# Kernel optimization log

Measured on AMD Instinct MI355X. Metric: run time of the kernel, lower is better.

## Reference

```python
import jax, jax.numpy as jnp
import numpy as np

KERNEL = (7, 7)
NUM_CH = 4
EPS = 1e-06
ROPE_BASE = 10000.0


def _rel_dist():
    coords = [np.arange(k, dtype=np.float32) - k // 2 for k in KERNEL]
    g = np.meshgrid(*coords, indexing='ij')
    d = np.sqrt(sum(gi ** 2 for gi in g))
    return jnp.asarray(d.reshape(-1)), float(d.max())


def silu(x):
    return x * jax.nn.sigmoid(x)


def rmsnorm(x, w):
    rms = jnp.sqrt(jnp.mean(x * x, axis=-1, keepdims=True) + EPS)
    return x / rms * w


def apply_rope(x):
    # x: (B, L, H, D); positions run over dim -2 (matches torch default)
    H, D = x.shape[-2], x.shape[-1]
    half = D // 2
    pos = jnp.arange(H, dtype=jnp.float32)
    freqs = 1.0 / (ROPE_BASE ** (jnp.arange(half, dtype=x.dtype) / half))
    ang = pos[:, None] * freqs  # (H, half)
    cos, sin = jnp.cos(ang), jnp.sin(ang)
    x1, x2 = x[..., :half], x[..., half:2 * half]
    return jnp.concatenate([x1 * cos - x2 * sin, x1 * sin + x2 * cos], axis=-1)


def unfold2d(x):
    # x: (B, Hs, Ws, C) -> (B, Hs, Ws, k1*k2, C), row-major kernel order
    B, Hs, Ws, C = x.shape
    k1, k2 = KERNEL
    xp = jnp.pad(x, ((0, 0), ((k1 - 1) // 2, k1 // 2), ((k2 - 1) // 2, k2 // 2), (0, 0)))
    wins = [xp[:, i:i + Hs, j:j + Ws, :] for i in range(k1) for j in range(k2)]
    return jnp.stack(wins, axis=3)


def setup_inputs() -> dict:
    key = jax.random.key(0)
    ks = jax.random.split(key, 8)
    C = 256
    x = jax.random.normal(ks[0], (2, 64, 64, C), dtype=jnp.float32)
    W_qkv = jax.random.normal(ks[1], (C, 3 * C), dtype=jnp.float32) * 0.02
    w_qnorm = jnp.ones((C // NUM_CH,), dtype=jnp.float32)
    w_knorm = jnp.ones((C // NUM_CH,), dtype=jnp.float32)
    W_wp = jax.random.normal(ks[2], (C, 2 * NUM_CH), dtype=jnp.float32) * 0.02
    b_wp = jax.random.normal(ks[3], (2 * NUM_CH,), dtype=jnp.float32) * 0.02
    w_onorm = jnp.ones((C,), dtype=jnp.float32)
    W_out = jax.random.normal(ks[4], (C, C), dtype=jnp.float32) * 0.02
    W_gate = jax.random.normal(ks[5], (C, C), dtype=jnp.float32) * 0.02
    b_gate = 2.0 * jnp.ones((C,), dtype=jnp.float32)
    return {"x": x, "W_qkv": W_qkv, "w_qnorm": w_qnorm, "w_knorm": w_knorm,
            "W_wp": W_wp, "b_wp": b_wp, "w_onorm": w_onorm, "W_out": W_out,
            "W_gate": W_gate, "b_gate": b_gate}


def reference(x, W_qkv, w_qnorm, w_knorm, W_wp, b_wp, w_onorm, W_out, W_gate, b_gate):
    rel_dist, max_dist = _rel_dist()
    B, Hs, Ws, C = x.shape
    L = Hs * Ws
    H = NUM_CH
    D = C // H
    Wsz = KERNEL[0] * KERNEL[1]
    scale = D ** (-0.5)

    qkv = silu(x @ W_qkv)
    q, k, v = jnp.split(qkv, 3, axis=-1)

    q_flat = apply_rope(rmsnorm(q.reshape(B, L, H, D), w_qnorm))
    k_flat = apply_rope(rmsnorm(k.reshape(B, L, H, D), w_knorm))
    k = k_flat.reshape(B, Hs, Ws, C)

    wp = silu(x @ W_wp + b_wp)  # (B, Hs, Ws, 2H)
    width_raw, sharp_raw = jnp.split(wp, 2, axis=-1)
    width = jax.nn.sigmoid(width_raw) * max_dist + 0.5
    sharpness = jax.nn.sigmoid(sharp_raw) * 9.5 + 0.5

    k_win = unfold2d(k).reshape(B, L, Wsz, H, D)
    v_win = unfold2d(v).reshape(B, L, Wsz, H, D)

    scores = jnp.einsum('blhd,blwhd->blhw', q_flat, k_win) * scale
    width_f = width.reshape(B, L, H, 1)
    sharp_f = sharpness.reshape(B, L, H, 1)
    soft_mask = jax.nn.sigmoid((width_f - rel_dist) * sharp_f)
    scores = scores - (1.0 - soft_mask) * 10000.0
    attn = jax.nn.softmax(scores, axis=-1)

    out = jnp.einsum('blhw,blwhd->blhd', attn, v_win).reshape(B, Hs, Ws, C)
    out = rmsnorm(out, w_onorm)

    gate = jax.nn.sigmoid(silu(v @ W_gate + b_gate))
    merged = gate * v + (1.0 - gate) * out
    return silu(merged @ W_out)
```

## Files before the change

kernel.cpp:

```cpp
#include <hip/hip_runtime.h>
#include <hip/hip_fp16.h>
#include <math.h>

__device__ __forceinline__ float sigm(float x)  { return 1.0f / (1.0f + __expf(-x)); }
__device__ __forceinline__ float siluf(float x) { return x * sigm(x); }

typedef _Float16 half8  __attribute__((ext_vector_type(8)));
typedef _Float16 half4  __attribute__((ext_vector_type(4)));
typedef float    f32x4  __attribute__((ext_vector_type(4)));

__device__ __forceinline__ void gld16(const void* g, void* l) {
    __builtin_amdgcn_global_load_lds(
        (const __attribute__((address_space(1))) unsigned*)g,
        (__attribute__((address_space(3))) unsigned*)l, 16, 0, 0);
}

template <int N>
__device__ __forceinline__ void wait_vmcnt() {
    if constexpr (N == 0)      asm volatile("s_waitcnt vmcnt(0)" ::: "memory");
    else if constexpr (N == 5) asm volatile("s_waitcnt vmcnt(5)" ::: "memory");
    else if constexpr (N == 6) asm volatile("s_waitcnt vmcnt(6)" ::: "memory");
}

template <int MI, int AMODE>
__device__ __forceinline__ void gemm_core16(
    const __half* __restrict__ A16,
    const __half* __restrict__ Bhi, const __half* __restrict__ Blo,
    int nbs, int m0, int n0, int t, f32x4 (&acc)[MI][4])
{
    __shared__ short As[2][MI * 1024], BsHi[2][4096], BsLo[2][4096];
    const int lane = t & 63, wave = t >> 6;
    const int wm = (wave >> 1) * (MI << 4), wn = (wave & 1) << 6;
    const int fr = lane & 15, fq = lane >> 4;
    constexpr int NL = MI / 2 + 4;

    auto stage = [&](int kb, int buf) {
#pragma unroll
        for (int hf = 0; hf < MI / 2; ++hf) {
            const int rr = wave * (MI << 3) + (hf << 4);
            size_t ga;
            if (AMODE == 0)
                ga = (((size_t)(kb * 8192 + m0 + rr)) << 5) + (lane << 3);
            else
                ga = (((size_t)(m0 + rr + (lane >> 2))) << 8) + (kb << 5) + ((lane & 3) << 3);
            gld16(A16 + ga, &As[buf][rr << 5]);
        }
#pragma unroll
        for (int hf = 0; hf < 2; ++hf) {
            const int rr = (wave << 5) + (hf << 4);
            const size_t gb = (((size_t)(kb * nbs + n0 + rr)) << 5) + (lane << 3);
            gld16(Bhi + gb, &BsHi[buf][rr << 5]);
            gld16(Blo + gb, &BsLo[buf][rr << 5]);
        }
    };

    stage(0, 0);
#pragma unroll
    for (int kb = 0; kb < 8; ++kb) {
        const int cur = kb & 1;
        if (kb < 7) {
            stage(kb + 1, cur ^ 1);
            wait_vmcnt<NL>();
        } else {
            wait_vmcnt<0>();
        }
        __builtin_amdgcn_s_barrier();

        half8 a[MI], bh[4], bl[4];
#pragma unroll
        for (int i = 0; i < MI; ++i)
            a[i] = *(const half8*)&As[cur][((wm + (i << 4) + fr) << 5) + (fq << 3)];
#pragma unroll
        for (int i = 0; i < 4; ++i) {
            const int boff = ((wn + (i << 4) + fr) << 5) + (fq << 3);
            bh[i] = *(const half8*)&BsHi[cur][boff];
            bl[i] = *(const half8*)&BsLo[cur][boff];
        }
#pragma unroll
        for (int mi = 0; mi < MI; ++mi)
#pragma unroll
            for (int ni = 0; ni < 4; ++ni) {
                acc[mi][ni] = __builtin_amdgcn_mfma_f32_16x16x32_f16(a[mi], bh[ni], acc[mi][ni], 0, 0, 0);
                acc[mi][ni] = __builtin_amdgcn_mfma_f32_16x16x32_f16(a[mi], bl[ni], acc[mi][ni], 0, 0, 0);
            }

        if (kb < 7) __builtin_amdgcn_s_barrier();
    }
}

__global__ __launch_bounds__(256) void prep_kernel(
    const float* __restrict__ x, const float* __restrict__ Wqkv,
    const float* __restrict__ Wgate, const float* __restrict__ Wout,
    const float* __restrict__ Wwp, const float* __restrict__ bwp,
    __half* __restrict__ xh,
    __half* __restrict__ wqh, __half* __restrict__ wql,
    __half* __restrict__ wgh, __half* __restrict__ wgl,
    __half* __restrict__ woh, __half* __restrict__ wol,
    float* __restrict__ width, float* __restrict__ sharp)
{
    __shared__ float xs[32][260];
    const int t = threadIdx.x;
    const int blk = blockIdx.x;
    if (blk < 256) {
        const int row0 = blk << 5;
        for (int e = t; e < 2048; e += 256) {
            int r = e >> 6, cc = (e & 63) << 2;
            *(float4*)&xs[r][cc] = *(const float4*)&x[(size_t)(row0 + r) * 256 + cc];
        }
        __syncthreads();
        const int r = t >> 3, kb = t & 7;
        __half hibuf[32];
#pragma unroll
        for (int i = 0; i < 32; ++i)
            hibuf[i] = __float2half(xs[r][(kb << 5) + i]);
        const size_t ob = ((size_t)(kb * 8192 + row0 + r)) << 5;
#pragma unroll
        for (int i = 0; i < 4; ++i)
            *(int4*)&xh[ob + (i << 3)] = *(int4*)&hibuf[i << 3];
        float a0 = 0.f, a1 = 0.f, a2 = 0.f, a3 = 0.f;
#pragma unroll 4
        for (int k = 0; k < 256; k += 4) {
            a0 += xs[r][k + 0] * Wwp[(k + 0) * 8 + kb];
            a1 += xs[r][k + 1] * Wwp[(k + 1) * 8 + kb];
            a2 += xs[r][k + 2] * Wwp[(k + 2) * 8 + kb];
            a3 += xs[r][k + 3] * Wwp[(k + 3) * 8 + kb];
        }
        const float acc = (a0 + a1) + (a2 + a3);
        float s = sigm(siluf(acc + bwp[kb]));
        const int row = row0 + r;
        if (kb < 4) width[row * 4 + kb] = s * 4.242640687119285f + 0.5f;
        else        sharp[row * 4 + kb - 4] = s * 9.5f + 0.5f;
    } else {
        const float* W; __half *Whi, *Wlo; int N, nb0, ncnt;
        if (blk < 288)      { W = Wqkv;  Whi = wqh; Wlo = wql; N = 768; nb0 = (blk - 256) * 24; ncnt = 24; }
        else if (blk < 296) { W = Wgate; Whi = wgh; Wlo = wgl; N = 256; nb0 = (blk - 288) * 32; ncnt = 32; }
        else                { W = Wout;  Whi = woh; Wlo = wol; N = 256; nb0 = (blk - 296) * 32; ncnt = 32; }
        for (int j = 0; j < ncnt; ++j)
            xs[j][t] = W[(size_t)t * N + nb0 + j];
        __syncthreads();
        for (int c = t; c < ncnt * 8; c += 256) {
            const int j = c >> 3, kb = c & 7;
            __half hibuf[32], lobuf[32];
#pragma unroll
            for (int i = 0; i < 32; ++i) {
                float v = xs[j][(kb << 5) + i];
                __half hv = __float2half(v);
                hibuf[i] = hv;
                lobuf[i] = __float2half(v - __half2float(hv));
            }
            const size_t ob = ((size_t)(kb * N + nb0 + j)) << 5;
#pragma unroll
            for (int i = 0; i < 4; ++i) {
                *(int4*)&Whi[ob + (i << 3)] = *(int4*)&hibuf[i << 3];
                *(int4*)&Wlo[ob + (i << 3)] = *(int4*)&lobuf[i << 3];
            }
        }
    }
}

__global__ __launch_bounds__(256, 3) void gemm_qkv(
    const __half* __restrict__ xh,
    const __half* __restrict__ wqh, const __half* __restrict__ wql,
    const float* __restrict__ wq, const float* __restrict__ wk,
    __half* __restrict__ qh, __half* __restrict__ kh, __half* __restrict__ vh)
{
    const int t  = threadIdx.x;
    const int m0 = blockIdx.y << 6, n0 = blockIdx.x << 7;
    f32x4 acc[2][4] = {};
    gemm_core16<2, 0>(xh, wqh, wql, 768, m0, n0, t, acc);

    const int lane = t & 63, wave = t >> 6;
    const int wm = (wave >> 1) << 5, wn = (wave & 1) << 6;
    const int fr = lane & 15, fq = lane >> 4;
    const int gc0 = n0 + wn;
    const int seg = gc0 >> 8;
    const int h   = (gc0 >> 6) & 3;
    const int hc0 = h << 6;

#pragma unroll
    for (int mi = 0; mi < 2; ++mi)
#pragma unroll
        for (int ni = 0; ni < 4; ++ni)
#pragma unroll
            for (int r = 0; r < 4; ++r)
                acc[mi][ni][r] = siluf(acc[mi][ni][r]);

    if (seg == 2) {
#pragma unroll
        for (int mi = 0; mi < 2; ++mi)
#pragma unroll
            for (int r = 0; r < 4; ++r) {
                const size_t row = m0 + wm + (mi << 4) + (fq << 2) + r;
#pragma unroll
                for (int ni = 0; ni < 4; ++ni)
                    vh[row * 256 + hc0 + (ni << 4) + fr] = __float2half(acc[mi][ni][r]);
            }
    } else {
        const float* wnorm = seg ? wk : wq;
        float wv[4];
#pragma unroll
        for (int ni = 0; ni < 4; ++ni) wv[ni] = wnorm[(ni << 4) + fr];
        float cs[2], sn[2];
#pragma unroll
        for (int j = 0; j < 2; ++j) {
            const int d = (j << 4) + fr;
            const float freq = powf(10000.f, -(float)d * (1.f / 32.f));
            const float ang = (float)h * freq;
            cs[j] = cosf(ang); sn[j] = sinf(ang);
        }
        __half* dstbase = (seg ? kh : qh);
#pragma unroll
        for (int mi = 0; mi < 2; ++mi)
#pragma unroll
            for (int r = 0; r < 4; ++r) {
                float ss = acc[mi][0][r] * acc[mi][0][r] + acc[mi][1][r] * acc[mi][1][r]
                         + acc[mi][2][r] * acc[mi][2][r] + acc[mi][3][r] * acc[mi][3][r];
                ss += __shfl_xor(ss, 1); ss += __shfl_xor(ss, 2);
                ss += __shfl_xor(ss, 4); ss += __shfl_xor(ss, 8);
                const float rinv = 1.f / sqrtf(ss * (1.f / 64.f) + 1e-6f);
                float xv[4];
#pragma unroll
                for (int ni = 0; ni < 4; ++ni) xv[ni] = acc[mi][ni][r] * rinv * wv[ni];
                const float o0 = xv[0] * cs[0] - xv[2] * sn[0];
                const float o2 = xv[0] * sn[0] + xv[2] * cs[0];
                const float o1 = xv[1] * cs[1] - xv[3] * sn[1];
                const float o3 = xv[1] * sn[1] + xv[3] * cs[1];
                const size_t row = m0 + wm + (mi << 4) + (fq << 2) + r;
                __half* dst = dstbase + row * 256 + hc0;
                dst[fr]      = __float2half(o0);
                dst[16 + fr] = __float2half(o1);
                dst[32 + fr] = __float2half(o2);
                dst[48 + fr] = __float2half(o3);
            }
    }
}

__global__ __launch_bounds__(256, 3) void gemm_gate(
    const __half* __restrict__ vh,
    const __half* __restrict__ wgh, const __half* __restrict__ wgl,
    const float* __restrict__ bias, const float* __restrict__ attn_o,
    const float* __restrict__ sumsq4, const float* __restrict__ w_onorm,
    __half* __restrict__ mh)
{
    const int t  = threadIdx.x;
    const int m0 = blockIdx.y << 6, n0 = blockIdx.x << 7;
    f32x4 acc[2][4] = {};
    gemm_core16<2, 1>(vh, wgh, wgl, 256, m0, n0, t, acc);

    const int lane = t & 63, wave = t >> 6;
    const int wm = (wave >> 1) << 5, wn = (wave & 1) << 6;
    const int fr = lane & 15, fq = lane >> 4;

    float rmsf[2][4];
#pragma unroll
    for (int mi = 0; mi < 2; ++mi)
#pragma unroll
        for (int r = 0; r < 4; ++r) {
            const int m = m0 + wm + (mi << 4) + (fq << 2) + r;
            float4 s4 = *(const float4*)&sumsq4[(size_t)m * 4];
            rmsf[mi][r] = 1.f / sqrtf((s4.x + s4.y + s4.z + s4.w) * (1.f / 256.f) + 1e-6f);
        }

#pragma unroll
    for (int mi = 0; mi < 2; ++mi)
#pragma unroll
        for (int ni = 0; ni < 4; ++ni) {
            const int n  = n0 + wn + (ni << 4) + fr;
            const int mb = m0 + wm + (mi << 4) + (fq << 2);
            const float bb  = bias[n];
            const float won = w_onorm[n];
#pragma unroll
            for (int r = 0; r < 4; ++r) {
                const int m = mb + r;
                const float g  = sigm(siluf(acc[mi][ni][r] + bb));
                const float vv = __half2float(vh[(size_t)m * 256 + n]);
                const float oo = attn_o[(size_t)m * 256 + n] * rmsf[mi][r] * won;
                mh[(size_t)m * 256 + n] = __float2half(g * vv + (1.f - g) * oo);
            }
        }
}

__global__ __launch_bounds__(256, 3) void gemm_out(
    const __half* __restrict__ mh,
    const __half* __restrict__ woh, const __half* __restrict__ wol,
    float* __restrict__ out)
{
    const int t  = threadIdx.x;
    const int m0 = blockIdx.y << 6, n0 = blockIdx.x << 7;
    f32x4 acc[2][4] = {};
    gemm_core16<2, 1>(mh, woh, wol, 256, m0, n0, t, acc);

    const int lane = t & 63, wave = t >> 6;
    const int wm = (wave >> 1) << 5, wn = (wave & 1) << 6;
    const int fr = lane & 15, fq = lane >> 4;
#pragma unroll
    for (int mi = 0; mi < 2; ++mi)
#pragma unroll
        for (int ni = 0; ni < 4; ++ni) {
            const int n  = n0 + wn + (ni << 4) + fr;
            const int mb = m0 + wm + (mi << 4) + (fq << 2);
#pragma unroll
            for (int r = 0; r < 4; ++r)
                out[(size_t)(mb + r) * 256 + n] = siluf(acc[mi][ni][r]);
        }
}

#define PT 216

__global__ __launch_bounds__(256, 2) void attn_mfma(
    const __half* __restrict__ qh, const __half* __restrict__ kh,
    const __half* __restrict__ vh, const float* __restrict__ width,
    const float* __restrict__ sharp, float* __restrict__ attn_o,
    float* __restrict__ sumsq4)
{
    __shared__ short smem[27648];
    short* Ksh = smem;
    short* Psh = smem;
    short* Vt  = smem + 13824;

    const int t = threadIdx.x;
    const int lane = t & 63, wave = t >> 6;
    const int fr = lane & 15, fq = lane >> 4;
    const int patch = blockIdx.x, h = blockIdx.y, b = blockIdx.z;
    const int pr0 = (patch >> 3) << 3, pc0 = (patch & 7) << 3;
    const int t0 = (wave * 28) >> 4;

    float wd[4], sh[4]; int lq[4];
#pragma unroll
    for (int r = 0; r < 4; ++r) {
        const int q = (wave << 4) + (fq << 2) + r;
        lq[r] = (pr0 + (q >> 3)) * 64 + pc0 + (q & 7);
        wd[r] = width[((b << 12) + lq[r]) * 4 + h];
        sh[r] = sharp[((b << 12) + lq[r]) * 4 + h];
    }

    const int qrow = (wave << 4) + fr;
    const int lqr = (pr0 + (qrow >> 3)) * 64 + pc0 + (qrow & 7);
    const __half* qptr = qh + (((size_t)(b << 12) + lqr) << 8) + (h << 6) + (fq << 3);
    half8 a0 = *(const half8*)qptr;
    half8 a1 = *(const half8*)(qptr + 32);

    const int srow = t >> 5;
    const int d2 = (t & 31) << 1;
    const size_t cbase = (((size_t)b << 12) * 256) + (size_t)h * 64 + d2;

    unsigned kb[25], vb[25];
#pragma unroll
    for (int p5 = 0; p5 < 25; ++p5) {
        const int prow = p5 * 8 + srow;
        const int pi = prow / 14, pj = prow - pi * 14;
        const int gr = pr0 - 3 + pi, gc = pc0 - 3 + pj;
        const bool ok = (prow < 196) & ((unsigned)gr < 64u) & ((unsigned)gc < 64u);
        const int grc = min(max(gr, 0), 63), gcc = min(max(gc, 0), 63);
        const size_t off = cbase + (size_t)(grc * 64 + gcc) * 256;
        unsigned kv = *(const unsigned*)(kh + off);
        unsigned vv = *(const unsigned*)(vh + off);
        kb[p5] = ok ? kv : 0u;
        vb[p5] = ok ? vv : 0u;
    }

    const int chunk = d2 >> 3, dlo = d2 & 7;
#pragma unroll
    for (int p5 = 0; p5 < 25; ++p5) {
        const int prow = p5 * 8 + srow;
        *(unsigned*)&Ksh[(prow << 6) + ((chunk ^ (prow & 7)) << 3) + dlo] = kb[p5];
        Vt[(d2)     * PT + prow] = (short)(vb[p5] & 0xffffu);
        Vt[(d2 + 1) * PT + prow] = (short)(vb[p5] >> 16);
    }
    if (t < 128) {
        const int rr = 200 + (t >> 4);
        *(unsigned*)&Ksh[(rr << 6) + (((t & 15) ^ ((rr & 7) << 1)) << 2)] = 0u;
    }
    for (int i = t; i < 64 * 20; i += 256)
        Vt[(i / 20) * PT + 196 + (i % 20)] = 0;
    __syncthreads();

    f32x4 sc[8];
#pragma unroll
    for (int tl = 0; tl < 8; ++tl) {
        const int kr = ((t0 + tl) << 4) + fr;
        half8 b0 = *(const half8*)&Ksh[(kr << 6) + (((0 + fq) ^ (kr & 7)) << 3)];
        half8 b1 = *(const half8*)&Ksh[(kr << 6) + (((4 + fq) ^ (kr & 7)) << 3)];
        f32x4 z = {0.f, 0.f, 0.f, 0.f};
        z = __builtin_amdgcn_mfma_f32_16x16x32_f16(a0, b0, z, 0, 0, 0);
        sc[tl] = __builtin_amdgcn_mfma_f32_16x16x32_f16(a1, b1, z, 0, 0, 0);
    }

    float mx[4] = {-3e38f, -3e38f, -3e38f, -3e38f};
#pragma unroll
    for (int tl = 0; tl < 8; ++tl) {
        const int p = ((t0 + tl) << 4) + fr;
        const int pi = p / 14, pj = p - pi * 14;
        const bool pvld = p < 196;
#pragma unroll
        for (int r = 0; r < 4; ++r) {
            const int q = (wave << 4) + (fq << 2) + r;
            const int di = pi - 3 - ((q >> 3) & 7), dj = pj - 3 - (q & 7);
            const bool win = pvld & ((unsigned)(di + 3) <= 6u) & ((unsigned)(dj + 3) <= 6u);
            const float rel = sqrtf((float)(di * di + dj * dj));
            const float mk = sigm((wd[r] - rel) * sh[r]);
            float s = sc[tl][r] * 0.125f - (1.f - mk) * 10000.f;
            s = win ? s : -3e38f;
            sc[tl][r] = s;
            mx[r] = fmaxf(mx[r], s);
        }
    }
#pragma unroll
    for (int r = 0; r < 4; ++r) {
        mx[r] = fmaxf(mx[r], __shfl_xor(mx[r], 1));
        mx[r] = fmaxf(mx[r], __shfl_xor(mx[r], 2));
        mx[r] = fmaxf(mx[r], __shfl_xor(mx[r], 4));
        mx[r] = fmaxf(mx[r], __shfl_xor(mx[r], 8));
    }
    float sm[4] = {0.f, 0.f, 0.f, 0.f};
#pragma unroll
    for (int tl = 0; tl < 8; ++tl)
#pragma unroll
        for (int r = 0; r < 4; ++r) {
            const float e = __expf(sc[tl][r] - mx[r]);
            sc[tl][r] = e; sm[r] += e;
        }
#pragma unroll
    for (int r = 0; r < 4; ++r) {
        sm[r] += __shfl_xor(sm[r], 1);
        sm[r] += __shfl_xor(sm[r], 2);
        sm[r] += __shfl_xor(sm[r], 4);
        sm[r] += __shfl_xor(sm[r], 8);
        sm[r] = 1.f / sm[r];
    }

    __syncthreads();
#pragma unroll
    for (int tl = 0; tl < 8; ++tl)
#pragma unroll
        for (int r = 0; r < 4; ++r) {
            __half pv = __float2half(sc[tl][r] * sm[r]);
            Psh[((wave << 4) + (fq << 2) + r) * PT + ((t0 + tl) << 4) + fr] = *(short*)&pv;
        }
    __syncthreads();

    f32x4 o[4] = {};
    const int pra = (wave << 4) + fr;
    const int cb = t0 << 4;
#pragma unroll
    for (int s = 0; s < 4; ++s) {
        half8 pa = *(const half8*)&Psh[pra * PT + cb + (fq << 3) + (s << 5)];
#pragma unroll
        for (int dt = 0; dt < 4; ++dt) {
            half8 vbf = *(const half8*)&Vt[((dt << 4) + fr) * PT + cb + (fq << 3) + (s << 5)];
            o[dt] = __builtin_amdgcn_mfma_f32_16x16x32_f16(pa, vbf, o[dt], 0, 0, 0);
        }
    }

#pragma unroll
    for (int r = 0; r < 4; ++r) {
        float ss = o[0][r]*o[0][r] + o[1][r]*o[1][r] + o[2][r]*o[2][r] + o[3][r]*o[3][r];
        ss += __shfl_xor(ss, 1); ss += __shfl_xor(ss, 2);
        ss += __shfl_xor(ss, 4); ss += __shfl_xor(ss, 8);
        const size_t rowb = (((size_t)(b << 12) + lq[r]) << 8) + h * 64;
#pragma unroll
        for (int dt = 0; dt < 4; ++dt)
            attn_o[rowb + (dt << 4) + fr] = o[dt][r];
        if (fr == 0) sumsq4[(((b << 12) + lq[r]) << 2) + h] = ss;
    }
}

extern "C" void kernel_launch(void* const* d_in, const int* in_sizes, int n_in,
                              void* d_out, int out_size, void* d_ws, size_t ws_size,
                              hipStream_t stream)
{
    const float* x      = (const float*)d_in[0];
    const float* W_qkv  = (const float*)d_in[1];
    const float* w_qn   = (const float*)d_in[2];
    const float* w_kn   = (const float*)d_in[3];
    const float* W_wp   = (const float*)d_in[4];
    const float* b_wp   = (const float*)d_in[5];
    const float* w_on   = (const float*)d_in[6];
    const float* W_out  = (const float*)d_in[7];
    const float* W_gate = (const float*)d_in[8];
    const float* b_gate = (const float*)d_in[9];
    float* out = (float*)d_out;

    __half* ws16 = (__half*)d_ws;
    __half* xh  = ws16;
    __half* wqh = xh  + 2097152;
    __half* wql = wqh + 196608;
    __half* wgh = wql + 196608;
    __half* wgl = wgh + 65536;
    __half* woh = wgl + 65536;
    __half* wol = woh + 65536;
    __half* qhp = wol + 65536;
    __half* khp = qhp + 2097152;
    __half* vhp = khp + 2097152;
    __half* mh  = vhp + 2097152;
    float* attn_o = (float*)(mh + 2097152);
    float* widthp = attn_o + 2097152;
    float* sharpp = widthp + 32768;
    float* sumsq4 = sharpp + 32768;

    prep_kernel<<<304, 256, 0, stream>>>(x, W_qkv, W_gate, W_out, W_wp, b_wp,
                                         xh, wqh, wql, wgh, wgl, woh, wol,
                                         widthp, sharpp);
    gemm_qkv<<<dim3(6, 128), 256, 0, stream>>>(xh, wqh, wql, w_qn, w_kn,
                                               qhp, khp, vhp);
    attn_mfma<<<dim3(64, 4, 2), 256, 0, stream>>>(qhp, khp, vhp, widthp, sharpp,
                                                  attn_o, sumsq4);
    gemm_gate<<<dim3(2, 128), 256, 0, stream>>>(vhp, wgh, wgl, b_gate,
                                                attn_o, sumsq4, w_on, mh);
    gemm_out<<<dim3(2, 128), 256, 0, stream>>>(mh, woh, wol, out);
}
```

Baseline: 136.1 us.

## Fuse gate and output GEMMs into one tail kernel with merged rows kept in LDS

Replaces the separate gate GEMM and output GEMM launches with one kernel. Each block handles 16 rows and computes the gate GEMM over all 256 columns, then writes the blended merged rows to shared memory as fp16 and runs the output GEMM from there. This removes one launch and the global round trip of the merged tensor. The cost is that every block restreams both full weight matrices, giving small 16-row tiles with lower MFMA reuse. It also changes the prep kernel's weight load to a coalesced transposed pattern.

```diff
diff --git a/kernel.cpp b/kernel.cpp
--- a/kernel.cpp
+++ b/kernel.cpp
@@ -18,6 +18,7 @@
 template <int N>
 __device__ __forceinline__ void wait_vmcnt() {
     if constexpr (N == 0)      asm volatile("s_waitcnt vmcnt(0)" ::: "memory");
+    else if constexpr (N == 4) asm volatile("s_waitcnt vmcnt(4)" ::: "memory");
     else if constexpr (N == 5) asm volatile("s_waitcnt vmcnt(5)" ::: "memory");
     else if constexpr (N == 6) asm volatile("s_waitcnt vmcnt(6)" ::: "memory");
 }
@@ -135,8 +136,10 @@
         if (blk < 288)      { W = Wqkv;  Whi = wqh; Wlo = wql; N = 768; nb0 = (blk - 256) * 24; ncnt = 24; }
         else if (blk < 296) { W = Wgate; Whi = wgh; Wlo = wgl; N = 256; nb0 = (blk - 288) * 32; ncnt = 32; }
         else                { W = Wout;  Whi = woh; Wlo = wol; N = 256; nb0 = (blk - 296) * 32; ncnt = 32; }
-        for (int j = 0; j < ncnt; ++j)
-            xs[j][t] = W[(size_t)t * N + nb0 + j];
+        for (int c = t; c < ncnt * 256; c += 256) {
+            const int k = c / ncnt, n = c - k * ncnt;
+            xs[n][k] = W[(size_t)k * N + nb0 + n];
+        }
         __syncthreads();
         for (int c = t; c < ncnt * 8; c += 256) {
             const int j = c >> 3, kb = c & 7;
@@ -235,73 +238,111 @@
     }
 }
 
-__global__ __launch_bounds__(256, 3) void gemm_gate(
+__global__ __launch_bounds__(256, 2) void gemm_tail(
     const __half* __restrict__ vh,
     const __half* __restrict__ wgh, const __half* __restrict__ wgl,
+    const __half* __restrict__ woh, const __half* __restrict__ wol,
     const float* __restrict__ bias, const float* __restrict__ attn_o,
     const float* __restrict__ sumsq4, const float* __restrict__ w_onorm,
-    __half* __restrict__ mh)
-{
-    const int t  = threadIdx.x;
-    const int m0 = blockIdx.y << 6, n0 = blockIdx.x << 7;
-    f32x4 acc[2][4] = {};
-    gemm_core16<2, 1>(vh, wgh, wgl, 256, m0, n0, t, acc);
-
-    const int lane = t & 63, wave = t >> 6;
-    const int wm = (wave >> 1) << 5, wn = (wave & 1) << 6;
-    const int fr = lane & 15, fq = lane >> 4;
-
-    float rmsf[2][4];
-#pragma unroll
-    for (int mi = 0; mi < 2; ++mi)
-#pragma unroll
-        for (int r = 0; r < 4; ++r) {
-            const int m = m0 + wm + (mi << 4) + (fq << 2) + r;
-            float4 s4 = *(const float4*)&sumsq4[(size_t)m * 4];
-            rmsf[mi][r] = 1.f / sqrtf((s4.x + s4.y + s4.z + s4.w) * (1.f / 256.f) + 1e-6f);
-        }
-
-#pragma unroll
-    for (int mi = 0; mi < 2; ++mi)
-#pragma unroll
-        for (int ni = 0; ni < 4; ++ni) {
-            const int n  = n0 + wn + (ni << 4) + fr;
-            const int mb = m0 + wm + (mi << 4) + (fq << 2);
-            const float bb  = bias[n];
-            const float won = w_onorm[n];
-#pragma unroll
-            for (int r = 0; r < 4; ++r) {
-                const int m = mb + r;
-                const float g  = sigm(siluf(acc[mi][ni][r] + bb));
-                const float vv = __half2float(vh[(size_t)m * 256 + n]);
-                const float oo = attn_o[(size_t)m * 256 + n] * rmsf[mi][r] * won;
-                mh[(size_t)m * 256 + n] = __float2half(g * vv + (1.f - g) * oo);
-            }
-        }
-}
-
-__global__ __launch_bounds__(256, 3) void gemm_out(
-    const __half* __restrict__ mh,
-    const __half* __restrict__ woh, const __half* __restrict__ wol,
     float* __restrict__ out)
 {
-    const int t  = threadIdx.x;
-    const int m0 = blockIdx.y << 6, n0 = blockIdx.x << 7;
-    f32x4 acc[2][4] = {};
-    gemm_core16<2, 1>(mh, woh, wol, 256, m0, n0, t, acc);
-
+    __shared__ short As_all[4096];
+    __shared__ short Bh[2][4096], Bl[2][4096];
+    __shared__ short Msh[16 * 264];
+
+    const int t = threadIdx.x;
     const int lane = t & 63, wave = t >> 6;
-    const int wm = (wave >> 1) << 5, wn = (wave & 1) << 6;
     const int fr = lane & 15, fq = lane >> 4;
-#pragma unroll
-    for (int mi = 0; mi < 2; ++mi)
-#pragma unroll
-        for (int ni = 0; ni < 4; ++ni) {
-            const int n  = n0 + wn + (ni << 4) + fr;
-            const int mb = m0 + wm + (mi << 4) + (fq << 2);
+    const int m0 = blockIdx.x << 4;
+
+    auto stageT = [&](int i) {
+        const int ph = i >> 3, kb = i & 7;
+        const __half* Whi = (ph < 2) ? wgh : woh;
+        const __half* Wlo = (ph < 2) ? wgl : wol;
+        const int nh = (ph & 1) << 7;
+        const int buf = i & 1;
+#pragma unroll
+        for (int hf = 0; hf < 2; ++hf) {
+            const int rr = (wave << 5) + (hf << 4);
+            const size_t gb = (((size_t)(kb * 256 + nh + rr)) << 5) + (lane << 3);
+            gld16(Whi + gb, &Bh[buf][rr << 5]);
+            gld16(Wlo + gb, &Bl[buf][rr << 5]);
+        }
+    };
+
+    f32x4 acc[4][2] = {};
+
+    if (wave == 0) {
+#pragma unroll
+        for (int kb = 0; kb < 8; ++kb) {
+            const size_t ga = (((size_t)(m0 + (lane >> 2))) << 8) + (kb << 5) + ((lane & 3) << 3);
+            gld16(vh + ga, &As_all[kb << 9]);
+        }
+    }
+    stageT(0);
+
+#pragma unroll
+    for (int i = 0; i < 32; ++i) {
+        if (i < 31) { stageT(i + 1); wait_vmcnt<4>(); }
+        else        wait_vmcnt<0>();
+        __builtin_amdgcn_s_barrier();
+
+        const int ph = i >> 3, kb = i & 7, cur = i & 1;
+        half8 a;
+        if (ph < 2) a = *(const half8*)&As_all[(kb << 9) + (fr << 5) + (fq << 3)];
+        else        a = *(const half8*)&Msh[fr * 264 + (kb << 5) + (fq << 3)];
+        half8 bhf[2], blf[2];
+#pragma unroll
+        for (int ni = 0; ni < 2; ++ni) {
+            const int boff = (((wave << 5) + (ni << 4) + fr) << 5) + (fq << 3);
+            bhf[ni] = *(const half8*)&Bh[cur][boff];
+            blf[ni] = *(const half8*)&Bl[cur][boff];
+        }
+#pragma unroll
+        for (int ni = 0; ni < 2; ++ni) {
+            acc[ph][ni] = __builtin_amdgcn_mfma_f32_16x16x32_f16(a, bhf[ni], acc[ph][ni], 0, 0, 0);
+            acc[ph][ni] = __builtin_amdgcn_mfma_f32_16x16x32_f16(a, blf[ni], acc[ph][ni], 0, 0, 0);
+        }
+
+        if (i == 15) {
+            float rmsf[4];
+#pragma unroll
+            for (int r = 0; r < 4; ++r) {
+                const int m = m0 + (fq << 2) + r;
+                float4 s4 = *(const float4*)&sumsq4[(size_t)m * 4];
+                rmsf[r] = 1.f / sqrtf((s4.x + s4.y + s4.z + s4.w) * (1.f / 256.f) + 1e-6f);
+            }
+#pragma unroll
+            for (int half_ = 0; half_ < 2; ++half_)
+#pragma unroll
+                for (int ni = 0; ni < 2; ++ni) {
+                    const int n = (half_ << 7) + (wave << 5) + (ni << 4) + fr;
+                    const float bb  = bias[n];
+                    const float won = w_onorm[n];
+#pragma unroll
+                    for (int r = 0; r < 4; ++r) {
+                        const int m = m0 + (fq << 2) + r;
+                        const float g  = sigm(siluf(acc[half_][ni][r] + bb));
+                        const float vv = __half2float(vh[(size_t)m * 256 + n]);
+                        const float oo = attn_o[(size_t)m * 256 + n] * rmsf[r] * won;
+                        __half mg = __float2half(g * vv + (1.f - g) * oo);
+                        Msh[((fq << 2) + r) * 264 + n] = *(short*)&mg;
+                    }
+                }
+            asm volatile("s_waitcnt lgkmcnt(0)" ::: "memory");
+        }
+
+        if (i < 31) __builtin_amdgcn_s_barrier();
+    }
+
+#pragma unroll
+    for (int ph = 2; ph < 4; ++ph)
+#pragma unroll
+        for (int ni = 0; ni < 2; ++ni) {
+            const int n = ((ph - 2) << 7) + (wave << 5) + (ni << 4) + fr;
 #pragma unroll
             for (int r = 0; r < 4; ++r)
-                out[(size_t)(mb + r) * 256 + n] = siluf(acc[mi][ni][r]);
+                out[(size_t)(m0 + (fq << 2) + r) * 256 + n] = siluf(acc[ph][ni][r]);
         }
 }
 
@@ -505,7 +546,6 @@
                                                qhp, khp, vhp);
     attn_mfma<<<dim3(64, 4, 2), 256, 0, stream>>>(qhp, khp, vhp, widthp, sharpp,
                                                   attn_o, sumsq4);
-    gemm_gate<<<dim3(2, 128), 256, 0, stream>>>(vhp, wgh, wgl, b_gate,
-                                                attn_o, sumsq4, w_on, mh);
-    gemm_out<<<dim3(2, 128), 256, 0, stream>>>(mh, woh, wol, out);
-}
+    gemm_tail<<<512, 256, 0, stream>>>(vhp, wgh, wgl, woh, wol, b_gate,
+                                       attn_o, sumsq4, w_on, out);
+}
```

Result: slower. 143.2 us (+5.2%).
